# Kernel optimization log

Measured on AMD Instinct MI355X. Metric: run time of the kernel, lower is better.

The kernel has to match this reference:

```python
import jax, jax.numpy as jnp
import numpy as np

B, DIM, H, W = 4, 512, 64, 64
NH = 8
HD = DIM // NH  # 64
CS = 16         # TTT mini_batch_size
BASE_LR = 1.0
EPS_IN = 1e-6   # inner ttt LayerNorm / post_norm eps
EPS_OUT = 1e-5  # wrapper nn.LayerNorm eps


def _ln(x, g, b, eps):
    mu = x.mean(-1, keepdims=True)
    var = ((x - mu) ** 2).mean(-1, keepdims=True)
    return (x - mu) / jnp.sqrt(var + eps) * g + b


def _ln_l2_bwd(Z, tgt, g, b):
    # fused: d/dZ of 0.5*||LN(Z; g,b) - tgt||^2
    D = Z.shape[-1]
    mu = Z.mean(-1, keepdims=True)
    var = ((Z - mu) ** 2).mean(-1, keepdims=True)
    std = jnp.sqrt(var + EPS_IN)
    xh = (Z - mu) / std
    gxh = ((g * xh + b) - tgt) * g
    return (D * gxh - gxh.sum(-1, keepdims=True) - xh * (gxh * xh).sum(-1, keepdims=True)) / (D * std)


def _rope(x, L):
    # x: [B, nh, L, f], llama-style rotary, theta=10000
    inv = 1.0 / (10000.0 ** (jnp.arange(0, HD, 2, dtype=jnp.float32) / HD))
    fr = jnp.arange(L, dtype=jnp.float32)[:, None] * inv[None, :]
    emb = jnp.concatenate([fr, fr], axis=-1)  # [L, f]
    cos, sin = jnp.cos(emb), jnp.sin(emb)
    x1, x2 = jnp.split(x, 2, axis=-1)
    return x * cos + jnp.concatenate([-x2, x1], axis=-1) * sin


def setup_inputs() -> dict:
    key = jax.random.key(0)
    ks = jax.random.split(key, 8)
    r = lambda k, s: 0.02 * jax.random.normal(k, s, dtype=jnp.float32)
    return {
        "x": jax.random.normal(ks[0], (B, DIM, H, W), dtype=jnp.float32),
        "ln_w": jnp.ones((DIM,), jnp.float32), "ln_b": jnp.zeros((DIM,), jnp.float32),
        "q_w": r(ks[1], (DIM, DIM)), "k_w": r(ks[2], (DIM, DIM)),
        "v_w": r(ks[3], (DIM, DIM)), "o_w": r(ks[4], (DIM, DIM)),
        "W1": r(ks[5], (NH, HD, HD)), "b1": jnp.zeros((NH, 1, HD), jnp.float32),
        "ttt_ln_w": jnp.ones((NH, HD), jnp.float32), "ttt_ln_b": jnp.zeros((NH, HD), jnp.float32),
        "lr_w": r(ks[6], (NH, 1, DIM)), "lr_b": jnp.zeros((NH, 1, 1), jnp.float32),
        "tok_idx_delta": jnp.zeros((CS,), jnp.float32),
        "post_w": jnp.ones((DIM,), jnp.float32), "post_b": jnp.zeros((DIM,), jnp.float32),
    }


def _ttt_linear(xn, q_w, k_w, v_w, o_w, W1, b1, ttt_ln_w, ttt_ln_b, lr_w, lr_b, tok_idx_delta, post_w, post_b):
    Bsz, L, _ = xn.shape
    NC = L // CS
    heads = lambda t: t.reshape(Bsz, L, NH, HD).transpose(0, 2, 1, 3)  # [B,nh,L,f]
    XQ = _rope(heads(xn @ q_w.T), L)
    XK = _rope(heads(xn @ k_w.T), L)
    XV = heads(xn @ v_w.T)

    # per-token learning rates eta: [B,nh,NC,CS,CS]
    Xc = xn.reshape(Bsz, NC, CS, DIM)
    ttt_lr = jax.nn.sigmoid(jnp.einsum("bnkc,hdc->bhnkd", Xc, lr_w) + lr_b.reshape(1, NH, 1, 1, 1))
    ttt_lr_eta = (BASE_LR / HD) * ttt_lr.transpose(0, 1, 2, 4, 3)  # [B,nh,NC,1,CS]
    token_idx = jnp.maximum(1.0 / jnp.arange(1, CS + 1, dtype=jnp.float32) + tok_idx_delta, 0.0)
    eta = token_idx.reshape(1, 1, 1, CS, 1) * ttt_lr_eta  # [B,nh,NC,CS,CS]

    g = ttt_ln_w[None, :, None, :]   # [1,nh,1,f]
    bb = ttt_ln_b[None, :, None, :]

    def step(carry, inp):
        W1c, b1c = carry                       # [B,nh,f,f], [B,nh,1,f]
        xq, xk, xv, et = inp                   # [B,nh,CS,f], eta [B,nh,CS,CS]
        Z1 = xk @ W1c + b1c
        grad = _ln_l2_bwd(Z1, xv - xk, g, bb)  # [B,nh,CS,f]
        Attn1 = jnp.tril(xq @ xk.swapaxes(-1, -2))
        b1_bar = b1c - jnp.tril(et) @ grad
        Z1_bar = xq @ W1c - (et * Attn1) @ grad + b1_bar
        last_eta = et[..., -1, :, None]        # [B,nh,CS,1]
        W1n = W1c - (last_eta * xk).swapaxes(-1, -2) @ grad
        b1n = b1c - (last_eta * grad).sum(-2, keepdims=True)
        return (W1n, b1n), xq + _ln(Z1_bar, g, bb, EPS_IN)

    W1_0 = jnp.broadcast_to(W1[None], (Bsz, NH, HD, HD)) + 0.0
    b1_0 = jnp.broadcast_to(b1[None], (Bsz, NH, 1, HD)) + 0.0
    chunk = lambda t: t.reshape(Bsz, NH, NC, CS, HD).transpose(2, 0, 1, 3, 4)
    _, out = jax.lax.scan(step, (W1_0, b1_0),
                          (chunk(XQ), chunk(XK), chunk(XV), eta.transpose(2, 0, 1, 3, 4)))
    # [NC,B,nh,CS,f] -> [B,L,D]
    out = out.transpose(1, 2, 0, 3, 4).reshape(Bsz, NH, L, HD).transpose(0, 2, 1, 3).reshape(Bsz, L, DIM)
    return _ln(out, post_w, post_b, EPS_IN) @ o_w.T


def reference(x, ln_w, ln_b, q_w, k_w, v_w, o_w, W1, b1, ttt_ln_w, ttt_ln_b, lr_w, lr_b, tok_idx_delta, post_w, post_b):
    Bsz, d = x.shape[:2]
    n_tok = x.shape[2] * x.shape[3]
    xf = x.reshape(Bsz, d, n_tok).transpose(0, 2, 1)   # [B, L, D]
    xn = _ln(xf, ln_w, ln_b, EPS_OUT)
    y = _ttt_linear(xn, q_w, k_w, v_w, o_w, W1, b1, ttt_ln_w, ttt_ln_b, lr_w, lr_b, tok_idx_delta, post_w, post_b)
    return y.transpose(0, 2, 1).reshape(x.shape)
```

## Files before the change

kernel.cpp:

```cpp
#include <hip/hip_runtime.h>
#include <hip/hip_bf16.h>
#include <math.h>

#define L_TOK 4096
#define DIMC  512

static __device__ __forceinline__ float4 f4fma(float a, const float4 b, const float4 c) {
    return make_float4(fmaf(a, b.x, c.x), fmaf(a, b.y, c.y), fmaf(a, b.z, c.z), fmaf(a, b.w, c.w));
}

__global__ __launch_bounds__(256) void rope_table_kernel(float* __restrict__ ctab, float* __restrict__ stab) {
    int idx = blockIdx.x * 256 + threadIdx.x;
    if (idx >= L_TOK * 32) return;
    int t = idx >> 5, m = idx & 31;
    float inv = 1.0f / powf(10000.0f, (float)(2 * m) * (1.0f / 64.0f));
    float fr = (float)t * inv;
    ctab[idx] = cosf(fr);
    stab[idx] = sinf(fr);
}

__global__ __launch_bounds__(256) void ln_in_kernel(const float* __restrict__ x,
                                                    const float* __restrict__ w,
                                                    const float* __restrict__ bia,
                                                    float* __restrict__ xn) {
    __shared__ float tile[16][516];
    __shared__ float redA[4][16], redB[4][16];
    __shared__ float mu_s[16], rs_s[16];
    int blk = blockIdx.x;
    int b = blk >> 8;
    int t0 = (blk & 255) << 4;
    int tid = threadIdx.x;
    int tt = tid & 15, cg = tid >> 4;
    int wid = tid >> 6;
    const float* xp = x + (size_t)b * DIMC * L_TOK + t0 + tt;
    float sum = 0.0f, sq = 0.0f;
#pragma unroll
    for (int i = 0; i < 32; i++) {
        int c = cg + (i << 4);
        float v = xp[(size_t)c * L_TOK];
        tile[tt][c] = v;
        sum += v; sq += v * v;
    }
    sum += __shfl_xor(sum, 16); sum += __shfl_xor(sum, 32);
    sq  += __shfl_xor(sq, 16);  sq  += __shfl_xor(sq, 32);
    if ((tid & 63) < 16) { redA[wid][tt] = sum; redB[wid][tt] = sq; }
    __syncthreads();
    if (tid < 16) {
        float s = redA[0][tid] + redA[1][tid] + redA[2][tid] + redA[3][tid];
        float q = redB[0][tid] + redB[1][tid] + redB[2][tid] + redB[3][tid];
        float mu = s * (1.0f / 512.0f);
        mu_s[tid] = mu;
        rs_s[tid] = rsqrtf(q * (1.0f / 512.0f) - mu * mu + 1e-5f);
    }
    __syncthreads();
    int half = tid >> 7;
    int cc = (tid & 127) << 2;
    float4 wv = *(const float4*)&w[cc];
    float4 bv = *(const float4*)&bia[cc];
    float* xnp = xn + ((size_t)b * L_TOK + t0) * DIMC;
#pragma unroll
    for (int i = 0; i < 8; i++) {
        int rr = half + (i << 1);
        float mu = mu_s[rr], rs = rs_s[rr];
        float4 v = *(float4*)&tile[rr][cc];
        float4 o;
        o.x = fmaf((v.x - mu) * rs, wv.x, bv.x);
        o.y = fmaf((v.y - mu) * rs, wv.y, bv.y);
        o.z = fmaf((v.z - mu) * rs, wv.z, bv.z);
        o.w = fmaf((v.w - mu) * rs, wv.w, bv.w);
        *(float4*)&xnp[(size_t)rr * DIMC + cc] = o;
    }
}

__global__ __launch_bounds__(256) void lr_kernel(const float* __restrict__ xn,
                                                 const float* __restrict__ lrw,
                                                 const float* __restrict__ lrb,
                                                 float* __restrict__ lre) {
    int tid = threadIdx.x;
    int lane = tid & 63, wid = tid >> 6;
    int tok = blockIdx.x * 4 + wid;
    const float* xp = xn + (size_t)tok * DIMC + lane * 8;
    float4 a0 = *(const float4*)xp;
    float4 a1 = *(const float4*)(xp + 4);
    int bb = tok >> 12, t = tok & 4095;
#pragma unroll
    for (int h = 0; h < 8; h++) {
        const float* wp = lrw + h * DIMC + lane * 8;
        float4 w0 = *(const float4*)wp;
        float4 w1 = *(const float4*)(wp + 4);
        float s = a0.x * w0.x + a0.y * w0.y + a0.z * w0.z + a0.w * w0.w
                + a1.x * w1.x + a1.y * w1.y + a1.z * w1.z + a1.w * w1.w;
        s += __shfl_xor(s, 1); s += __shfl_xor(s, 2); s += __shfl_xor(s, 4);
        s += __shfl_xor(s, 8); s += __shfl_xor(s, 16); s += __shfl_xor(s, 32);
        if (lane == 0) {
            float v = s + lrb[h];
            lre[(size_t)(bb * 8 + h) * L_TOK + t] = (1.0f / 64.0f) / (1.0f + expf(-v));
        }
    }
}

__global__ __launch_bounds__(256) void qkv_gemm_kernel(const float* __restrict__ A,
                                                       const float* __restrict__ qw,
                                                       const float* __restrict__ kw,
                                                       const float* __restrict__ vw,
                                                       float* __restrict__ XQ,
                                                       float* __restrict__ XK,
                                                       float* __restrict__ XV) {
    __shared__ float As[16][136];
    __shared__ float Bs[16][68];
    int tid = threadIdx.x;
    int mt = blockIdx.x, nt = blockIdx.y;
    const float* wsel = (nt < 8) ? qw : (nt < 16) ? kw : vw;
    int h = nt & 7;
    int arow = tid >> 1, ak = (tid & 1) << 3;
    int brow = tid >> 2, bk = (tid & 3) << 2;
    int tm8 = (tid >> 4) << 3, tn = tid & 15;
    float acc[8][4] = {};
    const float* ap = A + (size_t)(mt * 128 + arow) * DIMC + ak;
    const float* bp = wsel + (size_t)(h * 64 + brow) * DIMC + bk;
    for (int k0 = 0; k0 < DIMC; k0 += 16) {
        float4 a0 = *(const float4*)(ap + k0);
        float4 a1 = *(const float4*)(ap + k0 + 4);
        float4 bv = *(const float4*)(bp + k0);
        As[ak + 0][arow] = a0.x; As[ak + 1][arow] = a0.y; As[ak + 2][arow] = a0.z; As[ak + 3][arow] = a0.w;
        As[ak + 4][arow] = a1.x; As[ak + 5][arow] = a1.y; As[ak + 6][arow] = a1.z; As[ak + 7][arow] = a1.w;
        Bs[bk + 0][brow] = bv.x; Bs[bk + 1][brow] = bv.y; Bs[bk + 2][brow] = bv.z; Bs[bk + 3][brow] = bv.w;
        __syncthreads();
#pragma unroll
        for (int kk = 0; kk < 16; kk++) {
            float4 va0 = *(const float4*)&As[kk][tm8];
            float4 va1 = *(const float4*)&As[kk][tm8 + 4];
            float4 vb  = *(const float4*)&Bs[kk][tn << 2];
            float aa[8] = {va0.x, va0.y, va0.z, va0.w, va1.x, va1.y, va1.z, va1.w};
            float bb[4] = {vb.x, vb.y, vb.z, vb.w};
#pragma unroll
            for (int i = 0; i < 8; i++)
#pragma unroll
                for (int j = 0; j < 4; j++)
                    acc[i][j] = fmaf(aa[i], bb[j], acc[i][j]);
        }
        __syncthreads();
    }
    int m0 = mt * 128 + tm8;
    int bb2 = m0 >> 12, t = m0 & 4095;
    float* dst = (nt < 8) ? XQ : (nt < 16) ? XK : XV;
    dst += ((size_t)(bb2 * 8 + h) * L_TOK + t) * 64 + (tn << 2);
#pragma unroll
    for (int i = 0; i < 8; i++)
        *(float4*)(dst + (size_t)i * 64) = make_float4(acc[i][0], acc[i][1], acc[i][2], acc[i][3]);
}

__global__ __launch_bounds__(256) void rope_kernel(float* __restrict__ XQ, float* __restrict__ XK,
                                                   const float* __restrict__ ctab,
                                                   const float* __restrict__ stab) {
    int idx = blockIdx.x * 256 + threadIdx.x;
    int d = idx & 31;
    int t = (idx >> 5) & 4095;
    int bh = (idx >> 17) & 31;
    int tensor = idx >> 22;
    float* p = (tensor ? XK : XQ) + ((size_t)bh * L_TOK + t) * 64;
    float c = ctab[(t << 5) + d], s = stab[(t << 5) + d];
    float x1 = p[d], x2 = p[d + 32];
    p[d] = x1 * c - x2 * s;
    p[d + 32] = x2 * c + x1 * s;
}

__global__ __launch_bounds__(256) void scan_kernel(const float* __restrict__ XQ,
                                                   const float* __restrict__ XK,
                                                   const float* __restrict__ XV,
                                                   const float* __restrict__ lre,
                                                   const float* __restrict__ tok_delta,
                                                   const float* __restrict__ W1i,
                                                   const float* __restrict__ b1i,
                                                   const float* __restrict__ tw,
                                                   const float* __restrict__ tb,
                                                   float* __restrict__ attn_out) {
    __shared__ float W1[64][64];
    __shared__ float b1v[64];
    __shared__ float xqs[2][16][68], xks[2][16][68], xvs[2][16][68];
    __shared__ float grads[16][68];
    __shared__ float etas[2][16];
    __shared__ float coefC[16][17];
    __shared__ float sj[16];
    int tid = threadIdx.x;
    int r = tid >> 4, dq = tid & 15, d0 = dq << 2;
    int bh = blockIdx.x, h = bh & 7, b = bh >> 3;
#pragma unroll
    for (int i = 0; i < 4; i++) {
        int c = r + (i << 4);
        *(float4*)&W1[c][d0] = *(const float4*)&W1i[(size_t)h * 4096 + c * 64 + d0];
    }
    if (r == 0) *(float4*)&b1v[d0] = *(const float4*)&b1i[h * 64 + d0];
    float4 gw = *(const float4*)&tw[h * 64 + d0];
    float4 bw = *(const float4*)&tb[h * 64 + d0];
    float tok_r = fmaxf(1.0f / (float)(r + 1) + tok_delta[r], 0.0f);
    float tok15 = fmaxf(1.0f / 16.0f + tok_delta[15], 0.0f);
    const size_t base = (size_t)bh * L_TOK * 64;
    {
        size_t off = base + (size_t)r * 64 + d0;
        *(float4*)&xqs[0][r][d0] = *(const float4*)(XQ + off);
        *(float4*)&xks[0][r][d0] = *(const float4*)(XK + off);
        *(float4*)&xvs[0][r][d0] = *(const float4*)(XV + off);
        if (tid < 16) etas[0][tid] = lre[(size_t)bh * L_TOK + tid];
    }
    __syncthreads();
    int cur = 0;
    for (int n = 0; n < 256; n++) {
        int np = (n < 255) ? n + 1 : 255;
        size_t poff = base + (size_t)np * 1024 + (size_t)r * 64 + d0;
        float4 pfq = *(const float4*)(XQ + poff);
        float4 pfk = *(const float4*)(XK + poff);
        float4 pfv = *(const float4*)(XV + poff);
        float pfe = 0.0f;
        if (tid < 16) pfe = lre[(size_t)bh * L_TOK + np * 16 + tid];

        float4 b1reg = *(float4*)&b1v[d0];
        float4 z  = b1reg;
        float4 z2 = b1reg;
        float att = 0.0f;
#pragma unroll
        for (int c4 = 0; c4 < 16; c4++) {
            int c = c4 << 2;
            float4 xkr = *(float4*)&xks[cur][r][c];
            float4 xqr = *(float4*)&xqs[cur][r][c];
            float4 xkq = *(float4*)&xks[cur][dq][c];
            float4 w0 = *(float4*)&W1[c + 0][d0];
            float4 w1 = *(float4*)&W1[c + 1][d0];
            float4 w2 = *(float4*)&W1[c + 2][d0];
            float4 w3 = *(float4*)&W1[c + 3][d0];
            att += xqr.x * xkq.x + xqr.y * xkq.y + xqr.z * xkq.z + xqr.w * xkq.w;
            z  = f4fma(xkr.x, w0, z);  z  = f4fma(xkr.y, w1, z);
            z  = f4fma(xkr.z, w2, z);  z  = f4fma(xkr.w, w3, z);
            z2 = f4fma(xqr.x, w0, z2); z2 = f4fma(xqr.y, w1, z2);
            z2 = f4fma(xqr.z, w2, z2); z2 = f4fma(xqr.w, w3, z2);
        }
        float s = z.x + z.y + z.z + z.w;
        s += __shfl_xor(s, 1); s += __shfl_xor(s, 2); s += __shfl_xor(s, 4); s += __shfl_xor(s, 8);
        float mu = s * (1.0f / 64.0f);
        float4 dz = make_float4(z.x - mu, z.y - mu, z.z - mu, z.w - mu);
        float q = dz.x * dz.x + dz.y * dz.y + dz.z * dz.z + dz.w * dz.w;
        q += __shfl_xor(q, 1); q += __shfl_xor(q, 2); q += __shfl_xor(q, 4); q += __shfl_xor(q, 8);
        float rstd = rsqrtf(q * (1.0f / 64.0f) + 1e-6f);
        float4 xh = make_float4(dz.x * rstd, dz.y * rstd, dz.z * rstd, dz.w * rstd);
        float4 xvv = *(float4*)&xvs[cur][r][d0];
        float4 xkk = *(float4*)&xks[cur][r][d0];
        float4 gxh;
        gxh.x = (fmaf(gw.x, xh.x, bw.x) - (xvv.x - xkk.x)) * gw.x;
        gxh.y = (fmaf(gw.y, xh.y, bw.y) - (xvv.y - xkk.y)) * gw.y;
        gxh.z = (fmaf(gw.z, xh.z, bw.z) - (xvv.z - xkk.z)) * gw.z;
        gxh.w = (fmaf(gw.w, xh.w, bw.w) - (xvv.w - xkk.w)) * gw.w;
        float s1 = gxh.x + gxh.y + gxh.z + gxh.w;
        s1 += __shfl_xor(s1, 1); s1 += __shfl_xor(s1, 2); s1 += __shfl_xor(s1, 4); s1 += __shfl_xor(s1, 8);
        float s2 = gxh.x * xh.x + gxh.y * xh.y + gxh.z * xh.z + gxh.w * xh.w;
        s2 += __shfl_xor(s2, 1); s2 += __shfl_xor(s2, 2); s2 += __shfl_xor(s2, 4); s2 += __shfl_xor(s2, 8);
        float cgr = rstd * (1.0f / 64.0f);
        float4 grad;
        grad.x = (64.0f * gxh.x - s1 - xh.x * s2) * cgr;
        grad.y = (64.0f * gxh.y - s1 - xh.y * s2) * cgr;
        grad.z = (64.0f * gxh.z - s1 - xh.z * s2) * cgr;
        grad.w = (64.0f * gxh.w - s1 - xh.w * s2) * cgr;
        *(float4*)&grads[r][d0] = grad;
        float ceta = etas[cur][dq];
        coefC[r][dq] = (dq <= r) ? tok_r * ceta * (1.0f + att) : 0.0f;
        if (r == 15) sj[dq] = tok15 * ceta;
        __syncthreads();

        int r4 = r << 2;
        float4 acc0 = make_float4(0, 0, 0, 0), acc1 = acc0, acc2 = acc0, acc3 = acc0, accb = acc0;
#pragma unroll
        for (int j = 0; j < 16; j++) {
            float4 gj = *(float4*)&grads[j][d0];
            float cj = coefC[r][j];
            float sjj = sj[j];
            float4 xk4 = *(float4*)&xks[cur][j][r4];
            z2 = f4fma(-cj, gj, z2);
            acc0 = f4fma(sjj * xk4.x, gj, acc0);
            acc1 = f4fma(sjj * xk4.y, gj, acc1);
            acc2 = f4fma(sjj * xk4.z, gj, acc2);
            acc3 = f4fma(sjj * xk4.w, gj, acc3);
            accb = f4fma(sjj, gj, accb);
        }
        float so = z2.x + z2.y + z2.z + z2.w;
        so += __shfl_xor(so, 1); so += __shfl_xor(so, 2); so += __shfl_xor(so, 4); so += __shfl_xor(so, 8);
        float mu2 = so * (1.0f / 64.0f);
        float4 dz2 = make_float4(z2.x - mu2, z2.y - mu2, z2.z - mu2, z2.w - mu2);
        float q2 = dz2.x * dz2.x + dz2.y * dz2.y + dz2.z * dz2.z + dz2.w * dz2.w;
        q2 += __shfl_xor(q2, 1); q2 += __shfl_xor(q2, 2); q2 += __shfl_xor(q2, 4); q2 += __shfl_xor(q2, 8);
        float rstd2 = rsqrtf(q2 * (1.0f / 64.0f) + 1e-6f);
        float4 xq4 = *(float4*)&xqs[cur][r][d0];
        float4 o;
        o.x = fmaf(dz2.x * rstd2, gw.x, bw.x) + xq4.x;
        o.y = fmaf(dz2.y * rstd2, gw.y, bw.y) + xq4.y;
        o.z = fmaf(dz2.z * rstd2, gw.z, bw.z) + xq4.z;
        o.w = fmaf(dz2.w * rstd2, gw.w, bw.w) + xq4.w;
        *(float4*)(attn_out + ((size_t)b * L_TOK + (size_t)n * 16 + r) * DIMC + h * 64 + d0) = o;

        {
            float4 w0 = *(float4*)&W1[r4 + 0][d0];
            *(float4*)&W1[r4 + 0][d0] = make_float4(w0.x - acc0.x, w0.y - acc0.y, w0.z - acc0.z, w0.w - acc0.w);
            float4 w1 = *(float4*)&W1[r4 + 1][d0];
            *(float4*)&W1[r4 + 1][d0] = make_float4(w1.x - acc1.x, w1.y - acc1.y, w1.z - acc1.z, w1.w - acc1.w);
            float4 w2 = *(float4*)&W1[r4 + 2][d0];
            *(float4*)&W1[r4 + 2][d0] = make_float4(w2.x - acc2.x, w2.y - acc2.y, w2.z - acc2.z, w2.w - acc2.w);
            float4 w3 = *(float4*)&W1[r4 + 3][d0];
            *(float4*)&W1[r4 + 3][d0] = make_float4(w3.x - acc3.x, w3.y - acc3.y, w3.z - acc3.z, w3.w - acc3.w);
        }
        if (r == 0)
            *(float4*)&b1v[d0] = make_float4(b1reg.x - accb.x, b1reg.y - accb.y, b1reg.z - accb.z, b1reg.w - accb.w);

        int nxt = cur ^ 1;
        *(float4*)&xqs[nxt][r][d0] = pfq;
        *(float4*)&xks[nxt][r][d0] = pfk;
        *(float4*)&xvs[nxt][r][d0] = pfv;
        if (tid < 16) etas[nxt][tid] = pfe;
        __syncthreads();
        cur ^= 1;
    }
}

__global__ __launch_bounds__(256) void post_ln_kernel(float* __restrict__ at,
                                                      const float* __restrict__ w,
                                                      const float* __restrict__ b) {
    __shared__ float redA[4], redB[4];
    int row = blockIdx.x, tid = threadIdx.x;
    float* p = at + (size_t)row * DIMC;
    float v0 = p[tid], v1 = p[tid + 256];
    float s = v0 + v1, q = v0 * v0 + v1 * v1;
    s += __shfl_xor(s, 1); s += __shfl_xor(s, 2); s += __shfl_xor(s, 4);
    s += __shfl_xor(s, 8); s += __shfl_xor(s, 16); s += __shfl_xor(s, 32);
    q += __shfl_xor(q, 1); q += __shfl_xor(q, 2); q += __shfl_xor(q, 4);
    q += __shfl_xor(q, 8); q += __shfl_xor(q, 16); q += __shfl_xor(q, 32);
    if ((tid & 63) == 0) { redA[tid >> 6] = s; redB[tid >> 6] = q; }
    __syncthreads();
    s = redA[0] + redA[1] + redA[2] + redA[3];
    q = redB[0] + redB[1] + redB[2] + redB[3];
    float mu = s * (1.0f / 512.0f);
    float rs = rsqrtf(q * (1.0f / 512.0f) - mu * mu + 1e-6f);
    p[tid]       = fmaf((v0 - mu) * rs, w[tid],       b[tid]);
    p[tid + 256] = fmaf((v1 - mu) * rs, w[tid + 256], b[tid + 256]);
}

__global__ __launch_bounds__(256) void out_gemm_kernel(const float* __restrict__ A,
                                                       const float* __restrict__ ow,
                                                       float* __restrict__ out) {
    __shared__ float As[16][68];
    __shared__ float Bs[16][68];
    int tid = threadIdx.x;
    int mt = blockIdx.x, nt = blockIdx.y;
    int lrow = tid >> 2, lk = (tid & 3) << 2;
    int tm = tid >> 4, tn = tid & 15;
    float acc[4][4] = {};
    const float* ap = A + (size_t)(mt * 64 + lrow) * DIMC + lk;
    const float* bp = ow + (size_t)(nt * 64 + lrow) * DIMC + lk;
    for (int k0 = 0; k0 < DIMC; k0 += 16) {
        float4 av = *(const float4*)(ap + k0);
        float4 bv = *(const float4*)(bp + k0);
        As[lk + 0][lrow] = av.x; As[lk + 1][lrow] = av.y; As[lk + 2][lrow] = av.z; As[lk + 3][lrow] = av.w;
        Bs[lk + 0][lrow] = bv.x; Bs[lk + 1][lrow] = bv.y; Bs[lk + 2][lrow] = bv.z; Bs[lk + 3][lrow] = bv.w;
        __syncthreads();
#pragma unroll
        for (int kk = 0; kk < 16; kk++) {
            float4 a = *(const float4*)&As[kk][tm << 2];
            float4 bq = *(const float4*)&Bs[kk][tn << 2];
            float aa[4] = {a.x, a.y, a.z, a.w};
            float bb[4] = {bq.x, bq.y, bq.z, bq.w};
#pragma unroll
            for (int i = 0; i < 4; i++)
#pragma unroll
                for (int j = 0; j < 4; j++)
                    acc[i][j] = fmaf(aa[i], bb[j], acc[i][j]);
        }
        __syncthreads();
    }
    int m0 = mt * 64 + (tm << 2);
    int bb2 = m0 >> 12, t = m0 & 4095;
    int n0 = nt * 64 + (tn << 2);
#pragma unroll
    for (int j = 0; j < 4; j++)
        *(float4*)(out + ((size_t)(bb2 * DIMC) + n0 + j) * L_TOK + t) =
            make_float4(acc[0][j], acc[1][j], acc[2][j], acc[3][j]);
}

extern "C" void kernel_launch(void* const* d_in, const int* in_sizes, int n_in,
                              void* d_out, int out_size, void* d_ws, size_t ws_size,
                              hipStream_t stream) {
    (void)in_sizes; (void)n_in; (void)out_size; (void)ws_size;
    const float* x       = (const float*)d_in[0];
    const float* ln_w    = (const float*)d_in[1];
    const float* ln_b    = (const float*)d_in[2];
    const float* q_w     = (const float*)d_in[3];
    const float* k_w     = (const float*)d_in[4];
    const float* v_w     = (const float*)d_in[5];
    const float* o_w     = (const float*)d_in[6];
    const float* W1      = (const float*)d_in[7];
    const float* b1      = (const float*)d_in[8];
    const float* ttt_w   = (const float*)d_in[9];
    const float* ttt_b   = (const float*)d_in[10];
    const float* lr_w    = (const float*)d_in[11];
    const float* lr_b    = (const float*)d_in[12];
    const float* tok_d   = (const float*)d_in[13];
    const float* post_w  = (const float*)d_in[14];
    const float* post_b  = (const float*)d_in[15];

    float* ws = (float*)d_ws;
    const size_t NTD = (size_t)4 * L_TOK * DIMC;
    float* xn   = ws;
    float* XQb  = ws + NTD;
    float* XKb  = ws + 2 * NTD;
    float* XVb  = (float*)d_out;
    float* lre  = ws + 3 * NTD;
    float* ctab = lre + 131072;
    float* stab = ctab + 131072;
    float* attn = xn;

    rope_table_kernel<<<512, 256, 0, stream>>>(ctab, stab);
    ln_in_kernel<<<1024, 256, 0, stream>>>(x, ln_w, ln_b, xn);
    lr_kernel<<<4096, 256, 0, stream>>>(xn, lr_w, lr_b, lre);
    {
        dim3 g(128, 24);
        qkv_gemm_kernel<<<g, 256, 0, stream>>>(xn, q_w, k_w, v_w, XQb, XKb, XVb);
    }
    rope_kernel<<<32768, 256, 0, stream>>>(XQb, XKb, ctab, stab);
    scan_kernel<<<32, 256, 0, stream>>>(XQb, XKb, XVb, lre, tok_d, W1, b1, ttt_w, ttt_b, attn);
    post_ln_kernel<<<16384, 256, 0, stream>>>(attn, post_w, post_b);
    {
        dim3 g(256, 8);
        out_gemm_kernel<<<g, 256, 0, stream>>>(attn, o_w, (float*)d_out);
    }
}
```

Before: 1.595 ms.

## Pack two head-scans per block and widen output GEMM tiles to 128 rows

Result: slower. 4.870 ms (+205.4%).

```diff
diff --git a/kernel.cpp b/kernel.cpp
--- a/kernel.cpp
+++ b/kernel.cpp
@@ -165,7 +165,7 @@
     p[d + 32] = x2 * c + x1 * s;
 }
 
-__global__ __launch_bounds__(256) void scan_kernel(const float* __restrict__ XQ,
+__global__ __launch_bounds__(512) void scan_kernel(const float* __restrict__ XQ,
                                                    const float* __restrict__ XK,
                                                    const float* __restrict__ XV,
                                                    const float* __restrict__ lre,
@@ -175,22 +175,24 @@
                                                    const float* __restrict__ tw,
                                                    const float* __restrict__ tb,
                                                    float* __restrict__ attn_out) {
-    __shared__ float W1[64][64];
-    __shared__ float b1v[64];
-    __shared__ float xqs[2][16][68], xks[2][16][68], xvs[2][16][68];
-    __shared__ float grads[16][68];
-    __shared__ float etas[2][16];
-    __shared__ float coefC[16][17];
-    __shared__ float sj[16];
+    __shared__ float W1[2][64][64];
+    __shared__ float b1v[2][64];
+    __shared__ float xqs[2][2][16][68], xks[2][2][16][68], xvs[2][2][16][68];
+    __shared__ float grads[2][16][68];
+    __shared__ float etas[2][2][16];
+    __shared__ float coefC[2][16][17];
+    __shared__ float sj[2][16];
     int tid = threadIdx.x;
-    int r = tid >> 4, dq = tid & 15, d0 = dq << 2;
-    int bh = blockIdx.x, h = bh & 7, b = bh >> 3;
+    int ch = tid >> 8;
+    int t  = tid & 255;
+    int r = t >> 4, dq = t & 15, d0 = dq << 2;
+    int bh = blockIdx.x * 2 + ch, h = bh & 7, b = bh >> 3;
 #pragma unroll
     for (int i = 0; i < 4; i++) {
         int c = r + (i << 4);
-        *(float4*)&W1[c][d0] = *(const float4*)&W1i[(size_t)h * 4096 + c * 64 + d0];
-    }
-    if (r == 0) *(float4*)&b1v[d0] = *(const float4*)&b1i[h * 64 + d0];
+        *(float4*)&W1[ch][c][d0] = *(const float4*)&W1i[(size_t)h * 4096 + c * 64 + d0];
+    }
+    if (r == 0) *(float4*)&b1v[ch][d0] = *(const float4*)&b1i[h * 64 + d0];
     float4 gw = *(const float4*)&tw[h * 64 + d0];
     float4 bw = *(const float4*)&tb[h * 64 + d0];
     float tok_r = fmaxf(1.0f / (float)(r + 1) + tok_delta[r], 0.0f);
@@ -198,10 +200,10 @@
     const size_t base = (size_t)bh * L_TOK * 64;
     {
         size_t off = base + (size_t)r * 64 + d0;
-        *(float4*)&xqs[0][r][d0] = *(const float4*)(XQ + off);
-        *(float4*)&xks[0][r][d0] = *(const float4*)(XK + off);
-        *(float4*)&xvs[0][r][d0] = *(const float4*)(XV + off);
-        if (tid < 16) etas[0][tid] = lre[(size_t)bh * L_TOK + tid];
+        *(float4*)&xqs[ch][0][r][d0] = *(const float4*)(XQ + off);
+        *(float4*)&xks[ch][0][r][d0] = *(const float4*)(XK + off);
+        *(float4*)&xvs[ch][0][r][d0] = *(const float4*)(XV + off);
+        if (t < 16) etas[ch][0][t] = lre[(size_t)bh * L_TOK + t];
     }
     __syncthreads();
     int cur = 0;
@@ -212,22 +214,22 @@
         float4 pfk = *(const float4*)(XK + poff);
         float4 pfv = *(const float4*)(XV + poff);
         float pfe = 0.0f;
-        if (tid < 16) pfe = lre[(size_t)bh * L_TOK + np * 16 + tid];
-
-        float4 b1reg = *(float4*)&b1v[d0];
+        if (t < 16) pfe = lre[(size_t)bh * L_TOK + np * 16 + t];
+
+        float4 b1reg = *(float4*)&b1v[ch][d0];
         float4 z  = b1reg;
         float4 z2 = b1reg;
         float att = 0.0f;
 #pragma unroll
         for (int c4 = 0; c4 < 16; c4++) {
             int c = c4 << 2;
-            float4 xkr = *(float4*)&xks[cur][r][c];
-            float4 xqr = *(float4*)&xqs[cur][r][c];
-            float4 xkq = *(float4*)&xks[cur][dq][c];
-            float4 w0 = *(float4*)&W1[c + 0][d0];
-            float4 w1 = *(float4*)&W1[c + 1][d0];
-            float4 w2 = *(float4*)&W1[c + 2][d0];
-            float4 w3 = *(float4*)&W1[c + 3][d0];
+            float4 xkr = *(float4*)&xks[ch][cur][r][c];
+            float4 xqr = *(float4*)&xqs[ch][cur][r][c];
+            float4 xkq = *(float4*)&xks[ch][cur][dq][c];
+            float4 w0 = *(float4*)&W1[ch][c + 0][d0];
+            float4 w1 = *(float4*)&W1[ch][c + 1][d0];
+            float4 w2 = *(float4*)&W1[ch][c + 2][d0];
+            float4 w3 = *(float4*)&W1[ch][c + 3][d0];
             att += xqr.x * xkq.x + xqr.y * xkq.y + xqr.z * xkq.z + xqr.w * xkq.w;
             z  = f4fma(xkr.x, w0, z);  z  = f4fma(xkr.y, w1, z);
             z  = f4fma(xkr.z, w2, z);  z  = f4fma(xkr.w, w3, z);
@@ -242,8 +244,8 @@
         q += __shfl_xor(q, 1); q += __shfl_xor(q, 2); q += __shfl_xor(q, 4); q += __shfl_xor(q, 8);
         float rstd = rsqrtf(q * (1.0f / 64.0f) + 1e-6f);
         float4 xh = make_float4(dz.x * rstd, dz.y * rstd, dz.z * rstd, dz.w * rstd);
-        float4 xvv = *(float4*)&xvs[cur][r][d0];
-        float4 xkk = *(float4*)&xks[cur][r][d0];
+        float4 xvv = *(float4*)&xvs[ch][cur][r][d0];
+        float4 xkk = *(float4*)&xks[ch][cur][r][d0];
         float4 gxh;
         gxh.x = (fmaf(gw.x, xh.x, bw.x) - (xvv.x - xkk.x)) * gw.x;
         gxh.y = (fmaf(gw.y, xh.y, bw.y) - (xvv.y - xkk.y)) * gw.y;
@@ -259,20 +261,20 @@
         grad.y = (64.0f * gxh.y - s1 - xh.y * s2) * cgr;
         grad.z = (64.0f * gxh.z - s1 - xh.z * s2) * cgr;
         grad.w = (64.0f * gxh.w - s1 - xh.w * s2) * cgr;
-        *(float4*)&grads[r][d0] = grad;
-        float ceta = etas[cur][dq];
-        coefC[r][dq] = (dq <= r) ? tok_r * ceta * (1.0f + att) : 0.0f;
-        if (r == 15) sj[dq] = tok15 * ceta;
+        *(float4*)&grads[ch][r][d0] = grad;
+        float ceta = etas[ch][cur][dq];
+        coefC[ch][r][dq] = (dq <= r) ? tok_r * ceta * (1.0f + att) : 0.0f;
+        if (r == 15) sj[ch][dq] = tok15 * ceta;
         __syncthreads();
 
         int r4 = r << 2;
         float4 acc0 = make_float4(0, 0, 0, 0), acc1 = acc0, acc2 = acc0, acc3 = acc0, accb = acc0;
 #pragma unroll
         for (int j = 0; j < 16; j++) {
-            float4 gj = *(float4*)&grads[j][d0];
-            float cj = coefC[r][j];
-            float sjj = sj[j];
-            float4 xk4 = *(float4*)&xks[cur][j][r4];
+            float4 gj = *(float4*)&grads[ch][j][d0];
+            float cj = coefC[ch][r][j];
+            float sjj = sj[ch][j];
+            float4 xk4 = *(float4*)&xks[ch][cur][j][r4];
             z2 = f4fma(-cj, gj, z2);
             acc0 = f4fma(sjj * xk4.x, gj, acc0);
             acc1 = f4fma(sjj * xk4.y, gj, acc1);
@@ -287,7 +289,7 @@
         float q2 = dz2.x * dz2.x + dz2.y * dz2.y + dz2.z * dz2.z + dz2.w * dz2.w;
         q2 += __shfl_xor(q2, 1); q2 += __shfl_xor(q2, 2); q2 += __shfl_xor(q2, 4); q2 += __shfl_xor(q2, 8);
         float rstd2 = rsqrtf(q2 * (1.0f / 64.0f) + 1e-6f);
-        float4 xq4 = *(float4*)&xqs[cur][r][d0];
+        float4 xq4 = *(float4*)&xqs[ch][cur][r][d0];
         float4 o;
         o.x = fmaf(dz2.x * rstd2, gw.x, bw.x) + xq4.x;
         o.y = fmaf(dz2.y * rstd2, gw.y, bw.y) + xq4.y;
@@ -296,23 +298,23 @@
         *(float4*)(attn_out + ((size_t)b * L_TOK + (size_t)n * 16 + r) * DIMC + h * 64 + d0) = o;
 
         {
-            float4 w0 = *(float4*)&W1[r4 + 0][d0];
-            *(float4*)&W1[r4 + 0][d0] = make_float4(w0.x - acc0.x, w0.y - acc0.y, w0.z - acc0.z, w0.w - acc0.w);
-            float4 w1 = *(float4*)&W1[r4 + 1][d0];
-            *(float4*)&W1[r4 + 1][d0] = make_float4(w1.x - acc1.x, w1.y - acc1.y, w1.z - acc1.z, w1.w - acc1.w);
-            float4 w2 = *(float4*)&W1[r4 + 2][d0];
-            *(float4*)&W1[r4 + 2][d0] = make_float4(w2.x - acc2.x, w2.y - acc2.y, w2.z - acc2.z, w2.w - acc2.w);
-            float4 w3 = *(float4*)&W1[r4 + 3][d0];
-            *(float4*)&W1[r4 + 3][d0] = make_float4(w3.x - acc3.x, w3.y - acc3.y, w3.z - acc3.z, w3.w - acc3.w);
+            float4 w0 = *(float4*)&W1[ch][r4 + 0][d0];
+            *(float4*)&W1[ch][r4 + 0][d0] = make_float4(w0.x - acc0.x, w0.y - acc0.y, w0.z - acc0.z, w0.w - acc0.w);
+            float4 w1 = *(float4*)&W1[ch][r4 + 1][d0];
+            *(float4*)&W1[ch][r4 + 1][d0] = make_float4(w1.x - acc1.x, w1.y - acc1.y, w1.z - acc1.z, w1.w - acc1.w);
+            float4 w2 = *(float4*)&W1[ch][r4 + 2][d0];
+            *(float4*)&W1[ch][r4 + 2][d0] = make_float4(w2.x - acc2.x, w2.y - acc2.y, w2.z - acc2.z, w2.w - acc2.w);
+            float4 w3 = *(float4*)&W1[ch][r4 + 3][d0];
+            *(float4*)&W1[ch][r4 + 3][d0] = make_float4(w3.x - acc3.x, w3.y - acc3.y, w3.z - acc3.z, w3.w - acc3.w);
         }
         if (r == 0)
-            *(float4*)&b1v[d0] = make_float4(b1reg.x - accb.x, b1reg.y - accb.y, b1reg.z - accb.z, b1reg.w - accb.w);
+            *(float4*)&b1v[ch][d0] = make_float4(b1reg.x - accb.x, b1reg.y - accb.y, b1reg.z - accb.z, b1reg.w - accb.w);
 
         int nxt = cur ^ 1;
-        *(float4*)&xqs[nxt][r][d0] = pfq;
-        *(float4*)&xks[nxt][r][d0] = pfk;
-        *(float4*)&xvs[nxt][r][d0] = pfv;
-        if (tid < 16) etas[nxt][tid] = pfe;
+        *(float4*)&xqs[ch][nxt][r][d0] = pfq;
+        *(float4*)&xks[ch][nxt][r][d0] = pfk;
+        *(float4*)&xvs[ch][nxt][r][d0] = pfv;
+        if (t < 16) etas[ch][nxt][t] = pfe;
         __syncthreads();
         cur ^= 1;
     }
@@ -343,42 +345,48 @@
 __global__ __launch_bounds__(256) void out_gemm_kernel(const float* __restrict__ A,
                                                        const float* __restrict__ ow,
                                                        float* __restrict__ out) {
-    __shared__ float As[16][68];
+    __shared__ float As[16][136];
     __shared__ float Bs[16][68];
     int tid = threadIdx.x;
     int mt = blockIdx.x, nt = blockIdx.y;
-    int lrow = tid >> 2, lk = (tid & 3) << 2;
-    int tm = tid >> 4, tn = tid & 15;
-    float acc[4][4] = {};
-    const float* ap = A + (size_t)(mt * 64 + lrow) * DIMC + lk;
-    const float* bp = ow + (size_t)(nt * 64 + lrow) * DIMC + lk;
+    int arow = tid >> 1, ak = (tid & 1) << 3;
+    int brow = tid >> 2, bk = (tid & 3) << 2;
+    int tm8 = (tid >> 4) << 3, tn = tid & 15;
+    float acc[8][4] = {};
+    const float* ap = A + (size_t)(mt * 128 + arow) * DIMC + ak;
+    const float* bp = ow + (size_t)(nt * 64 + brow) * DIMC + bk;
     for (int k0 = 0; k0 < DIMC; k0 += 16) {
-        float4 av = *(const float4*)(ap + k0);
+        float4 a0 = *(const float4*)(ap + k0);
+        float4 a1 = *(const float4*)(ap + k0 + 4);
         float4 bv = *(const float4*)(bp + k0);
-        As[lk + 0][lrow] = av.x; As[lk + 1][lrow] = av.y; As[lk + 2][lrow] = av.z; As[lk + 3][lrow] = av.w;
-        Bs[lk + 0][lrow] = bv.x; Bs[lk + 1][lrow] = bv.y; Bs[lk + 2][lrow] = bv.z; Bs[lk + 3][lrow] = bv.w;
+        As[ak + 0][arow] = a0.x; As[ak + 1][arow] = a0.y; As[ak + 2][arow] = a0.z; As[ak + 3][arow] = a0.w;
+        As[ak + 4][arow] = a1.x; As[ak + 5][arow] = a1.y; As[ak + 6][arow] = a1.z; As[ak + 7][arow] = a1.w;
+        Bs[bk + 0][brow] = bv.x; Bs[bk + 1][brow] = bv.y; Bs[bk + 2][brow] = bv.z; Bs[bk + 3][brow] = bv.w;
         __syncthreads();
 #pragma unroll
         for (int kk = 0; kk < 16; kk++) {
-            float4 a = *(const float4*)&As[kk][tm << 2];
-            float4 bq = *(const float4*)&Bs[kk][tn << 2];
-            float aa[4] = {a.x, a.y, a.z, a.w};
-            float bb[4] = {bq.x, bq.y, bq.z, bq.w};
-#pragma unroll
-            for (int i = 0; i < 4; i++)
+            float4 va0 = *(const float4*)&As[kk][tm8];
+            float4 va1 = *(const float4*)&As[kk][tm8 + 4];
+            float4 vb  = *(const float4*)&Bs[kk][tn << 2];
+            float aa[8] = {va0.x, va0.y, va0.z, va0.w, va1.x, va1.y, va1.z, va1.w};
+            float bb[4] = {vb.x, vb.y, vb.z, vb.w};
+#pragma unroll
+            for (int i = 0; i < 8; i++)
 #pragma unroll
                 for (int j = 0; j < 4; j++)
                     acc[i][j] = fmaf(aa[i], bb[j], acc[i][j]);
         }
         __syncthreads();
     }
-    int m0 = mt * 64 + (tm << 2);
+    int m0 = mt * 128 + tm8;
     int bb2 = m0 >> 12, t = m0 & 4095;
     int n0 = nt * 64 + (tn << 2);
 #pragma unroll
-    for (int j = 0; j < 4; j++)
-        *(float4*)(out + ((size_t)(bb2 * DIMC) + n0 + j) * L_TOK + t) =
-            make_float4(acc[0][j], acc[1][j], acc[2][j], acc[3][j]);
+    for (int j = 0; j < 4; j++) {
+        float* op = out + ((size_t)(bb2 * DIMC) + n0 + j) * L_TOK + t;
+        *(float4*)op       = make_float4(acc[0][j], acc[1][j], acc[2][j], acc[3][j]);
+        *(float4*)(op + 4) = make_float4(acc[4][j], acc[5][j], acc[6][j], acc[7][j]);
+    }
 }
 
 extern "C" void kernel_launch(void* const* d_in, const int* in_sizes, int n_in,
@@ -421,10 +429,10 @@
         qkv_gemm_kernel<<<g, 256, 0, stream>>>(xn, q_w, k_w, v_w, XQb, XKb, XVb);
     }
     rope_kernel<<<32768, 256, 0, stream>>>(XQb, XKb, ctab, stab);
-    scan_kernel<<<32, 256, 0, stream>>>(XQb, XKb, XVb, lre, tok_d, W1, b1, ttt_w, ttt_b, attn);
+    scan_kernel<<<16, 512, 0, stream>>>(XQb, XKb, XVb, lre, tok_d, W1, b1, ttt_w, ttt_b, attn);
     post_ln_kernel<<<16384, 256, 0, stream>>>(attn, post_w, post_b);
     {
-        dim3 g(256, 8);
+        dim3 g(128, 8);
         out_gemm_kernel<<<g, 256, 0, stream>>>(attn, o_w, (float*)d_out);
     }
 }
```
